# Kernel tuning notes

Hardware: AMD Instinct MI355X
Metric: run time of the kernel (lower is better)

Reference implementation:

```python
import jax, jax.numpy as jnp
import numpy as np

CHUNK = 32
FLOOR = 0.01
EPS_MIX = 1e-5
EPS_NORM = 1e-5


def l2norm(x):
    return x / jnp.sqrt(jnp.sum(x * x, -1, keepdims=True) + 1e-12)


def dw_causal_conv(x, w):
    # x: (B, L, C), w: (C, K) depthwise causal conv, tap K-1 is 'current'
    K = w.shape[-1]
    L = x.shape[1]
    xp = jnp.pad(x, ((0, 0), (K - 1, 0), (0, 0)))
    y = jnp.zeros_like(x)
    for t in range(K):
        y = y + xp[:, t:t + L, :] * w[:, t]
    return y


def delta_rule_chunkwise(q, k, v, beta):
    # q,k: (B,H,L,dk), v: (B,H,L,dv), beta: (B,H,L); L % CHUNK == 0
    b, h, L, dk = q.shape
    dv = v.shape[-1]
    c = CHUNK
    n = L // c
    q = l2norm(q)
    k = l2norm(k)
    v = v * beta[..., None]
    kb = k * beta[..., None]
    rs = lambda x: x.reshape(b, h, n, c, -1)
    qc, kc, vc, kbc = rs(q), rs(k), rs(v), rs(kb)
    # in-chunk inverse of (I + tril(K_beta K^T)) via forward substitution
    T = -jnp.einsum('bhnid,bhnjd->bhnij', kbc, kc)
    tri_strict = jnp.tril(jnp.ones((c, c), bool), -1)
    T = jnp.where(tri_strict, T, 0.0)
    for i in range(1, c):
        T = T.at[..., i, :i].add(
            jnp.einsum('bhnj,bhnji->bhni', T[..., i, :], T[..., :, :i]))
    T = T + jnp.eye(c, dtype=T.dtype)
    u = jnp.einsum('bhnij,bhnjd->bhnid', T, vc)
    w = jnp.einsum('bhnij,bhnjd->bhnid', T, kbc)
    mask_incl = jnp.tril(jnp.ones((c, c), bool), 0)

    def step(S, inp):
        qi, ki, ui, wi = inp  # each (b,h,c,d)
        attn = jnp.einsum('bhid,bhjd->bhij', qi, ki)
        attn = jnp.where(mask_incl, attn, 0.0)
        u_i = ui - jnp.einsum('bhik,bhkd->bhid', wi, S)
        o_i = jnp.einsum('bhik,bhkd->bhid', qi, S) + jnp.einsum('bhij,bhjd->bhid', attn, u_i)
        S = S + jnp.einsum('bhci,bhcd->bhid', ki, u_i)
        return S, o_i

    S0 = jnp.zeros((b, h, dk, dv), q.dtype)
    xs = tuple(jnp.moveaxis(a, 2, 0) for a in (qc, kc, u, w))
    S, o = jax.lax.scan(step, S0, xs)
    o = jnp.moveaxis(o, 0, 2).reshape(b, h, L, dv)
    return o, S


def setup_inputs() -> dict:
    key = jax.random.key(0)
    B, L, D, H = 4, 4096, 1024, 4
    dh = D // H  # 256
    ks = jax.random.split(key, 20)
    s = 1.0 / np.sqrt(D)
    inp = {
        'hidden_states': jax.random.normal(ks[0], (B, L, D), jnp.float32),
        'Wq': jax.random.normal(ks[1], (D, D), jnp.float32) * s,
        'Wk': jax.random.normal(ks[2], (D, D), jnp.float32) * s,
        'Wv': jax.random.normal(ks[3], (D, D), jnp.float32) * s,
        'Wb': jax.random.normal(ks[4], (D, H), jnp.float32) * s,
        'conv_q_w': jax.random.normal(ks[5], (D, 4), jnp.float32) * 0.5,
        'conv_k_w': jax.random.normal(ks[6], (D, 4), jnp.float32) * 0.5,
        'conv_v_w': jax.random.normal(ks[7], (D, 4), jnp.float32) * 0.5,
        'local_w': (jax.random.normal(ks[8], (H * dh, 7), jnp.float32) / np.sqrt(7.0)).at[:, -1].add(1.0),
        'mid_w': (jax.random.normal(ks[9], (H * dh, 25), jnp.float32) / np.sqrt(25.0)).at[:, -1].add(1.0),
        'r_w1': jax.random.normal(ks[10], (D + 14 * H, 2 * (D + 14 * H)), jnp.float32) / np.sqrt(D + 14 * H),
        'r_b1': jnp.zeros((2 * (D + 14 * H),), jnp.float32),
        'r_w2': jax.random.normal(ks[11], (2 * (D + 14 * H), H * 4), jnp.float32) / np.sqrt(2.0 * (D + 14 * H)),
        'r_b2': jnp.zeros((H, 4), jnp.float32).at[:, 2:].set(0.7).reshape(-1),
        'mix_w': jnp.ones((H, dh), jnp.float32),
        'onorm_w': jnp.ones((dh,), jnp.float32),
        'Wo': jax.random.normal(ks[12], (D, D), jnp.float32) * s,
    }
    return inp


def reference(hidden_states, Wq, Wk, Wv, Wb, conv_q_w, conv_k_w, conv_v_w,
              local_w, mid_w, r_w1, r_b1, r_w2, r_b2, mix_w, onorm_w, Wo):
    B, L, D = hidden_states.shape
    H = mix_w.shape[0]
    dh = mix_w.shape[1]
    # projections + short causal depthwise convs with SiLU (qk_activation='silu')
    q = jax.nn.silu(dw_causal_conv(hidden_states @ Wq, conv_q_w))
    k = jax.nn.silu(dw_causal_conv(hidden_states @ Wk, conv_k_w))
    v = jax.nn.silu(dw_causal_conv(hidden_states @ Wv, conv_v_w))
    q4 = q.reshape(B, L, H, dh)
    k4 = k.reshape(B, L, H, dh)
    v4 = v.reshape(B, L, H, dh)
    beta = jax.nn.sigmoid(hidden_states @ Wb)  # (B,L,H)
    delta_out, _ = delta_rule_chunkwise(
        jnp.transpose(q4, (0, 2, 1, 3)), jnp.transpose(k4, (0, 2, 1, 3)),
        jnp.transpose(v4, (0, 2, 1, 3)), jnp.transpose(beta, (0, 2, 1)))
    delta_out = jnp.transpose(delta_out, (0, 2, 1, 3))  # (B,L,H,dh)
    v_direct = v4
    vflat = v4.reshape(B, L, H * dh)
    local_out = dw_causal_conv(vflat, local_w).reshape(B, L, H, dh)
    mid_out = dw_causal_conv(vflat, mid_w).reshape(B, L, H, dh)
    outs = [local_out, mid_out, delta_out, v_direct]
    # router stats: per-head mean/var of each path + pairwise mean dots
    feats = []
    for o_ in outs:
        feats.append(o_.mean(-1))
        feats.append(jnp.var(o_, -1, ddof=1))
    for i in range(4):
        for j in range(i + 1, 4):
            feats.append((outs[i] * outs[j]).mean(-1))
    router_feat = jnp.concatenate([hidden_states] + feats, axis=-1)  # (B,L,D+14H)
    h1 = jax.nn.silu(router_feat @ r_w1 + r_b1)
    logits = (h1 @ r_w2 + r_b2).reshape(B, L, H, 4)
    p = jax.nn.softmax(logits, -1)
    p = p * (1.0 - 4.0 * FLOOR) + FLOOR  # probability floor
    mixed = sum(p[..., i:i + 1] * outs[i] for i in range(4))  # (B,L,H,dh)
    # MixNorm: per-token per-head RMSNorm with (H,dh) affine
    rms = jnp.sqrt(jnp.mean(mixed * mixed, -1, keepdims=True) + EPS_MIX)
    mixed = mixed / rms * mix_w
    # output RMSNorm (per head_v_dim)
    rms2 = jnp.sqrt(jnp.mean(mixed * mixed, -1, keepdims=True) + EPS_NORM)
    o_n = mixed / rms2 * onorm_w
    return o_n.reshape(B, L, H * dh) @ Wo
```

## Files before the change

kernel.cpp:

```cpp
#include <hip/hip_runtime.h>
#include <cstdint>
#include <cstddef>

typedef unsigned short u16;
typedef __bf16 bf16x8 __attribute__((ext_vector_type(8)));
typedef float    f32x4 __attribute__((ext_vector_type(4)));
typedef unsigned short u16x8 __attribute__((ext_vector_type(8)));
typedef unsigned short u16x4 __attribute__((ext_vector_type(4)));

#define MFMA16(a,b,c) __builtin_amdgcn_mfma_f32_16x16x32_bf16(a,b,c,0,0,0)

__device__ __forceinline__ float bf2f(u16 u){ return __uint_as_float(((unsigned)u)<<16); }
__device__ __forceinline__ u16 f2bf(float f){
  unsigned x = __float_as_uint(f);
  unsigned r = x + 0x7fffu + ((x>>16)&1u);
  return (u16)(r>>16);
}
__device__ __forceinline__ float wred(float v){
  #pragma unroll
  for (int o=32;o;o>>=1) v += __shfl_xor(v,o,64);
  return v;
}
__device__ __forceinline__ float siluf(float x){ return x/(1.f+__expf(-x)); }

__global__ __launch_bounds__(256) void k_zero(float* __restrict__ p, int n){
  int i = blockIdx.x*256 + threadIdx.x;
  if (i < n) p[i] = 0.f;
}

__global__ __launch_bounds__(256) void k_cvt(const float* __restrict__ src,
                                             u16* __restrict__ dst, int n){
  int i = (blockIdx.x*256 + threadIdx.x)*4;
  if (i < n){
    float4 f = *(const float4*)(src + i);
    u16x4 o; o[0]=f2bf(f.x); o[1]=f2bf(f.y); o[2]=f2bf(f.z); o[3]=f2bf(f.w);
    *(u16x4*)(dst + i) = o;
  }
}

__global__ __launch_bounds__(256) void k_tr(const float* __restrict__ src, u16* __restrict__ dst,
                                            int R, int C, int Rp, int Cp){
  __shared__ float t[32][33];
  int n0 = blockIdx.x*32, k0 = blockIdx.y*32;
  int tx = threadIdx.x & 31, ty = threadIdx.x >> 5;
  #pragma unroll
  for (int j=0;j<4;j++){
    int k = k0 + ty + j*8, nn = n0 + tx;
    t[ty + j*8][tx] = (k < R && nn < C) ? src[k*C + nn] : 0.f;
  }
  __syncthreads();
  #pragma unroll
  for (int j=0;j<4;j++){
    int nn = n0 + ty + j*8, k = k0 + tx;
    dst[nn*Rp + k] = f2bf(t[tx][ty + j*8]);
  }
}

__global__ __launch_bounds__(256) void k_pad_w2t(const float* __restrict__ src, u16* __restrict__ dst){
  int k = blockIdx.x*256 + threadIdx.x;
  int j = blockIdx.y;
  if (k < 2176) dst[j*2176 + k] = (k < 2160) ? f2bf(src[k*16 + j]) : (u16)0;
}
__global__ __launch_bounds__(256) void k_pad_b1(const float* __restrict__ src, float* __restrict__ dst){
  int i = blockIdx.x*256 + threadIdx.x;
  if (i < 2176) dst[i] = (i<2160) ? src[i] : 0.f;
}

__global__ __launch_bounds__(256,2) void k_gemm(
    const u16* __restrict__ A, const u16* __restrict__ Bt, void* __restrict__ Cvp,
    int M, int N, int K, int out_f32)
{
  __shared__ u16 As[2][128*64];
  __shared__ u16 Bs[2][128*64];
  const int tid = threadIdx.x;
  const int lane = tid & 63, wv = tid >> 6;
  const int wm = (wv>>1)*64, wn = (wv&1)*64;
  const int r15 = lane & 15, q4 = lane >> 4;
  const int bm0 = blockIdx.y*128, bn0 = blockIdx.x*128;
  const int srow = tid>>3, sch = tid&7;
  const int nk = K >> 6;

  const f32x4 fz = {0.f,0.f,0.f,0.f};
  f32x4 acc[4][4];
  #pragma unroll
  for (int i=0;i<4;i++){
    #pragma unroll
    for (int j=0;j<4;j++) acc[i][j] = fz;
  }

  {
    u16x8 ca[4], cb[4];
    #pragma unroll
    for (int i=0;i<4;i++){
      int r = i*32 + srow;
      ca[i] = *(const u16x8*)(A  + (size_t)(bm0+r)*K + sch*8);
      cb[i] = *(const u16x8*)(Bt + (size_t)(bn0+r)*K + sch*8);
    }
    #pragma unroll
    for (int i=0;i<4;i++){
      int r = i*32 + srow;
      int byt = r*128 + ((sch ^ (r&7))*16);
      *(u16x8*)((char*)(&As[0][0]) + byt) = ca[i];
      *(u16x8*)((char*)(&Bs[0][0]) + byt) = cb[i];
    }
  }
  int cur = 0;
  for (int t=0; t<nk; ++t){
    u16x8 na[4], nb[4];
    if (t+1 < nk){
      const int kt = (t+1)<<6;
      #pragma unroll
      for (int i=0;i<4;i++){
        int r = i*32 + srow;
        na[i] = *(const u16x8*)(A  + (size_t)(bm0+r)*K + kt + sch*8);
        nb[i] = *(const u16x8*)(Bt + (size_t)(bn0+r)*K + kt + sch*8);
      }
    }
    __syncthreads();
    const u16* as_ = &As[cur][0];
    const u16* bs_ = &Bs[cur][0];
    #pragma unroll
    for (int kk=0; kk<2; ++kk){
      bf16x8 av[4], bv[4];
      #pragma unroll
      for (int mi=0;mi<4;mi++){
        int row = wm + mi*16 + r15;
        int ch  = kk*4 + q4;
        av[mi] = *(const bf16x8*)((const char*)as_ + row*128 + ((ch ^ (row&7))*16));
      }
      #pragma unroll
      for (int ni=0;ni<4;ni++){
        int row = wn + ni*16 + r15;
        int ch  = kk*4 + q4;
        bv[ni] = *(const bf16x8*)((const char*)bs_ + row*128 + ((ch ^ (row&7))*16));
      }
      #pragma unroll
      for (int mi=0;mi<4;mi++){
        #pragma unroll
        for (int ni=0;ni<4;ni++)
          acc[mi][ni] = MFMA16(av[mi], bv[ni], acc[mi][ni]);
      }
    }
    if (t+1 < nk){
      #pragma unroll
      for (int i=0;i<4;i++){
        int r = i*32 + srow;
        int byt = r*128 + ((sch ^ (r&7))*16);
        *(u16x8*)((char*)(&As[cur^1][0]) + byt) = na[i];
        *(u16x8*)((char*)(&Bs[cur^1][0]) + byt) = nb[i];
      }
    }
    cur ^= 1;
  }
  float* Cf = (float*)Cvp;
  u16*  Cb2 = (u16*)Cvp;
  #pragma unroll
  for (int mi=0;mi<4;mi++){
    #pragma unroll
    for (int ni=0;ni<4;ni++){
      int gr = bm0 + wm + mi*16 + q4*4;
      int gc = bn0 + wn + ni*16 + r15;
      #pragma unroll
      for (int rg=0; rg<4; ++rg){
        float v = acc[mi][ni][rg];
        size_t off = (size_t)(gr+rg)*N + gc;
        if (out_f32) Cf[off] = v; else Cb2[off] = f2bf(v);
      }
    }
  }
}

union SMu {
  struct { u16 As[2][128*64]; u16 Bs[2][128*64]; } g;
  u16 h1s[128][136];
};
__global__ __launch_bounds__(256,2) void k_gemm_router(
    const u16* __restrict__ A, const u16* __restrict__ Bt,
    const float* __restrict__ bias, const u16* __restrict__ w2t,
    float* __restrict__ logits)
{
  __shared__ SMu sm;
  const int tid = threadIdx.x;
  const int lane = tid & 63, wv = tid >> 6;
  const int wm = (wv>>1)*64, wn = (wv&1)*64;
  const int r15 = lane & 15, q4 = lane >> 4;
  const int bm0 = blockIdx.y*128, bn0 = blockIdx.x*128;
  const int srow = tid>>3, sch = tid&7;
  const int K = 1088, nk = 17;

  const f32x4 fz = {0.f,0.f,0.f,0.f};
  f32x4 acc[4][4];
  #pragma unroll
  for (int i=0;i<4;i++){
    #pragma unroll
    for (int j=0;j<4;j++) acc[i][j] = fz;
  }
  {
    u16x8 ca[4], cb[4];
    #pragma unroll
    for (int i=0;i<4;i++){
      int r = i*32 + srow;
      ca[i] = *(const u16x8*)(A  + (size_t)(bm0+r)*K + sch*8);
      cb[i] = *(const u16x8*)(Bt + (size_t)(bn0+r)*K + sch*8);
    }
    #pragma unroll
    for (int i=0;i<4;i++){
      int r = i*32 + srow;
      int byt = r*128 + ((sch ^ (r&7))*16);
      *(u16x8*)((char*)(&sm.g.As[0][0]) + byt) = ca[i];
      *(u16x8*)((char*)(&sm.g.Bs[0][0]) + byt) = cb[i];
    }
  }
  int cur = 0;
  for (int t=0; t<nk; ++t){
    u16x8 na[4], nb[4];
    if (t+1 < nk){
      const int kt = (t+1)<<6;
      #pragma unroll
      for (int i=0;i<4;i++){
        int r = i*32 + srow;
        na[i] = *(const u16x8*)(A  + (size_t)(bm0+r)*K + kt + sch*8);
        nb[i] = *(const u16x8*)(Bt + (size_t)(bn0+r)*K + kt + sch*8);
      }
    }
    __syncthreads();
    const u16* as_ = &sm.g.As[cur][0];
    const u16* bs_ = &sm.g.Bs[cur][0];
    #pragma unroll
    for (int kk=0; kk<2; ++kk){
      bf16x8 av[4], bv[4];
      #pragma unroll
      for (int mi=0;mi<4;mi++){
        int row = wm + mi*16 + r15;
        int ch  = kk*4 + q4;
        av[mi] = *(const bf16x8*)((const char*)as_ + row*128 + ((ch ^ (row&7))*16));
      }
      #pragma unroll
      for (int ni=0;ni<4;ni++){
        int row = wn + ni*16 + r15;
        int ch  = kk*4 + q4;
        bv[ni] = *(const bf16x8*)((const char*)bs_ + row*128 + ((ch ^ (row&7))*16));
      }
      #pragma unroll
      for (int mi=0;mi<4;mi++){
        #pragma unroll
        for (int ni=0;ni<4;ni++)
          acc[mi][ni] = MFMA16(av[mi], bv[ni], acc[mi][ni]);
      }
    }
    if (t+1 < nk){
      #pragma unroll
      for (int i=0;i<4;i++){
        int r = i*32 + srow;
        int byt = r*128 + ((sch ^ (r&7))*16);
        *(u16x8*)((char*)(&sm.g.As[cur^1][0]) + byt) = na[i];
        *(u16x8*)((char*)(&sm.g.Bs[cur^1][0]) + byt) = nb[i];
      }
    }
    cur ^= 1;
  }
  __syncthreads();
  #pragma unroll
  for (int mi=0;mi<4;mi++){
    #pragma unroll
    for (int ni=0;ni<4;ni++){
      int lr = wm + mi*16 + q4*4;
      int lc = wn + ni*16 + r15;
      float bv_ = bias[bn0 + lc];
      #pragma unroll
      for (int rg=0; rg<4; ++rg)
        sm.h1s[lr+rg][lc] = f2bf(siluf(acc[mi][ni][rg] + bv_));
    }
  }
  __syncthreads();
  f32x4 lacc[2] = {fz, fz};
  #pragma unroll
  for (int rt=0; rt<2; ++rt){
    #pragma unroll
    for (int ks=0; ks<4; ++ks){
      bf16x8 a = *(const bf16x8*)((const char*)&sm.h1s[wv*32 + rt*16 + r15][0] + ks*64 + q4*16);
      bf16x8 b = *(const bf16x8*)(w2t + r15*2176 + bn0 + ks*32 + q4*8);
      lacc[rt] = MFMA16(a, b, lacc[rt]);
    }
  }
  #pragma unroll
  for (int rt=0; rt<2; ++rt){
    #pragma unroll
    for (int rg=0; rg<4; ++rg){
      int m = bm0 + wv*32 + rt*16 + q4*4 + rg;
      atomicAdd(&logits[m*16 + r15], lacc[rt][rg]);
    }
  }
}

__global__ __launch_bounds__(256) void k_softm(float* __restrict__ p, const float* __restrict__ b2){
  int m = blockIdx.x*256 + threadIdx.x;
  float l[16];
  #pragma unroll
  for (int j=0;j<16;j++) l[j] = p[m*16+j] + b2[j];
  #pragma unroll
  for (int hh=0;hh<4;hh++){
    float l0=l[hh*4+0], l1=l[hh*4+1], l2=l[hh*4+2], l3=l[hh*4+3];
    float mx = fmaxf(fmaxf(l0,l1),fmaxf(l2,l3));
    float e0=__expf(l0-mx), e1=__expf(l1-mx), e2=__expf(l2-mx), e3=__expf(l3-mx);
    float iv = 1.f/(e0+e1+e2+e3);
    p[m*16+hh*4+0]=e0*iv*0.96f+0.01f;
    p[m*16+hh*4+1]=e1*iv*0.96f+0.01f;
    p[m*16+hh*4+2]=e2*iv*0.96f+0.01f;
    p[m*16+hh*4+3]=e3*iv*0.96f+0.01f;
  }
}

__global__ __launch_bounds__(256) void k_beta(const u16* __restrict__ Xb,
                                              const float* __restrict__ Wb,
                                              float* __restrict__ beta){
  int m = blockIdx.x*4 + (threadIdx.x>>6);
  int lane = threadIdx.x & 63;
  float a0=0.f,a1=0.f,a2=0.f,a3=0.f;
  #pragma unroll 4
  for (int i=0;i<16;i++){
    int k = lane + i*64;
    float x = bf2f(Xb[m*1024 + k]);
    float4 wr = *(const float4*)(Wb + k*4);
    a0 += x*wr.x; a1 += x*wr.y; a2 += x*wr.z; a3 += x*wr.w;
  }
  a0 = wred(a0); a1 = wred(a1); a2 = wred(a2); a3 = wred(a3);
  if (lane == 0){
    beta[m*4+0] = 1.f/(1.f+__expf(-a0));
    beta[m*4+1] = 1.f/(1.f+__expf(-a1));
    beta[m*4+2] = 1.f/(1.f+__expf(-a2));
    beta[m*4+3] = 1.f/(1.f+__expf(-a3));
  }
}

__global__ __launch_bounds__(256) void k_conv(const u16* __restrict__ raw,
                                              const float* __restrict__ cw,
                                              u16* __restrict__ outp, int do_norm){
  const int m = blockIdx.x;
  const int tid = threadIdx.x, lane = tid&63, hh = tid>>6;
  const int l = m & 4095;
  const int cbase = hh*256 + lane*4;
  float x[4][4];
  #pragma unroll
  for (int j=0;j<4;j++){
    if (l >= j){
      u16x4 xv = *(const u16x4*)(raw + (m-j)*1024 + cbase);
      #pragma unroll
      for (int e=0;e<4;e++) x[j][e] = bf2f(xv[e]);
    } else {
      #pragma unroll
      for (int e=0;e<4;e++) x[j][e] = 0.f;
    }
  }
  float y[4]; float ss = 0.f;
  #pragma unroll
  for (int e=0;e<4;e++){
    int c = cbase + e;
    float yy = x[0][e]*cw[c*4+3] + x[1][e]*cw[c*4+2] + x[2][e]*cw[c*4+1] + x[3][e]*cw[c*4+0];
    yy = siluf(yy);
    y[e] = yy; ss += yy*yy;
  }
  if (do_norm){
    ss = wred(ss);
    float sc = rsqrtf(ss + 1e-12f);
    #pragma unroll
    for (int e=0;e<4;e++) y[e] *= sc;
  }
  u16x4 o;
  #pragma unroll
  for (int e=0;e<4;e++) o[e] = f2bf(y[e]);
  *(u16x4*)(outp + m*1024 + cbase) = o;
}

__global__ __launch_bounds__(256) void k_localmid(const u16* __restrict__ v,
                                                  const float* __restrict__ lw,
                                                  const float* __restrict__ mw,
                                                  u16* __restrict__ lo, u16* __restrict__ mo){
  __shared__ u16 vs[56][256];
  const int lt0 = blockIdx.x*32;
  const int b = blockIdx.y;
  const int c0 = blockIdx.z*256;
  const int tid = threadIdx.x;
  #pragma unroll
  for (int i=0;i<7;i++){
    int flat = tid + i*256;
    int row = flat >> 5;
    int cc = (flat & 31)*8;
    int tok = lt0 - 24 + row;
    u16x8 val = {0,0,0,0,0,0,0,0};
    if (tok >= 0) val = *(const u16x8*)(v + (b*4096 + tok)*1024 + c0 + cc);
    *(u16x8*)&vs[row][cc] = val;
  }
  __syncthreads();
  const int c = tid;
  float lwr[7], mwr[25];
  #pragma unroll
  for (int i=0;i<7;i++) lwr[i] = lw[(c0+c)*7 + i];
  #pragma unroll
  for (int i=0;i<25;i++) mwr[i] = mw[(c0+c)*25 + i];
  for (int lt=0; lt<32; ++lt){
    float a7=0.f, a25=0.f;
    #pragma unroll
    for (int t=0;t<25;t++) a25 += bf2f(vs[lt+t][c]) * mwr[t];
    #pragma unroll
    for (int t=0;t<7;t++)  a7  += bf2f(vs[18+lt+t][c]) * lwr[t];
    int m = b*4096 + lt0 + lt;
    lo[m*1024 + c0 + c] = f2bf(a7);
    mo[m*1024 + c0 + c] = f2bf(a25);
  }
}

__global__ __launch_bounds__(256,2) void k_chunk(
    const u16* __restrict__ qn, const u16* __restrict__ kn, const u16* __restrict__ v,
    const float* __restrict__ beta, u16* __restrict__ u_, u16* __restrict__ w_,
    u16* __restrict__ attnb)
{
  const int chk = blockIdx.x;
  const int nc = chk & 127;
  const int bh = chk >> 7;
  const int b = bh >> 2, h = bh & 3;
  const int tok0 = b*4096 + nc*32;
  const int tid = threadIdx.x, lane = tid&63, wv = tid>>6;
  const int r15 = lane&15, q4 = lane>>4;

  __shared__ u16 kbT[256][40];
  __shared__ u16 vbT[256][40];
  __shared__ float Tm[4][32][33];
  __shared__ u16 Xs[32][40];

  {
    int rr = tid >> 3;
    int cb = (tid & 7)*32;
    float bt = beta[(tok0 + rr)*4 + h];
    const u16* ksrc = kn + (tok0+rr)*1024 + h*256 + cb;
    const u16* vsrc = v  + (tok0+rr)*1024 + h*256 + cb;
    #pragma unroll
    for (int vvv=0; vvv<4; ++vvv){
      u16x8 kx = *(const u16x8*)(ksrc + vvv*8);
      u16x8 vx = *(const u16x8*)(vsrc + vvv*8);
      #pragma unroll
      for (int e=0;e<8;e++){
        kbT[cb + vvv*8 + e][rr] = f2bf(bf2f(kx[e]) * bt);
        vbT[cb + vvv*8 + e][rr] = f2bf(bf2f(vx[e]) * bt);
      }
    }
  }
  {
    const int i0 = (wv>>1)*16, j0 = (wv&1)*16;
    float bi = beta[(tok0 + i0 + r15)*4 + h];
    f32x4 tacc = {0.f,0.f,0.f,0.f};
    #pragma unroll
    for (int ks=0; ks<8; ++ks){
      u16x8 ar = *(const u16x8*)(kn + (tok0 + i0 + r15)*1024 + h*256 + ks*32 + q4*8);
      union { u16x8 u; bf16x8 bf; } au;
      #pragma unroll
      for (int e=0;e<8;e++) au.u[e] = f2bf(bf2f(ar[e]) * bi);
      bf16x8 bv = *(const bf16x8*)(kn + (tok0 + j0 + r15)*1024 + h*256 + ks*32 + q4*8);
      tacc = MFMA16(au.bf, bv, tacc);
    }
    #pragma unroll
    for (int rg=0; rg<4; ++rg){
      int i = i0 + q4*4 + rg, j = j0 + r15;
      float val = (i > j) ? -tacc[rg] : 0.f;
      Tm[0][i][j] = val;
      Tm[2][i][j] = val + ((i==j)?1.f:0.f);
    }
  }
  __syncthreads();
  int cbuf = 0, cx = 2;
  const int ii = tid >> 3, jj = (tid&7)*4;
  for (int s=0; s<4; ++s){
    int nb = cbuf^1, nx = cx^1;
    {
      float o0=0.f,o1=0.f,o2=0.f,o3=0.f;
      for (int k=0;k<32;k++){
        float a = Tm[cbuf][ii][k];
        o0 += a*Tm[cbuf][k][jj+0]; o1 += a*Tm[cbuf][k][jj+1];
        o2 += a*Tm[cbuf][k][jj+2]; o3 += a*Tm[cbuf][k][jj+3];
      }
      Tm[nb][ii][jj+0]=o0; Tm[nb][ii][jj+1]=o1; Tm[nb][ii][jj+2]=o2; Tm[nb][ii][jj+3]=o3;
    }
    __syncthreads();
    {
      float o0=Tm[cx][ii][jj+0], o1=Tm[cx][ii][jj+1], o2=Tm[cx][ii][jj+2], o3=Tm[cx][ii][jj+3];
      for (int k=0;k<32;k++){
        float a = Tm[nb][ii][k];
        o0 += a*Tm[cx][k][jj+0]; o1 += a*Tm[cx][k][jj+1];
        o2 += a*Tm[cx][k][jj+2]; o3 += a*Tm[cx][k][jj+3];
      }
      Tm[nx][ii][jj+0]=o0; Tm[nx][ii][jj+1]=o1; Tm[nx][ii][jj+2]=o2; Tm[nx][ii][jj+3]=o3;
    }
    __syncthreads();
    cbuf = nb; cx = nx;
  }
  {
    #pragma unroll
    for (int e=0;e<4;e++) Xs[ii][jj+e] = f2bf(Tm[cx][ii][jj+e]);
  }
  __syncthreads();
  {
    #pragma unroll
    for (int nt=0; nt<4; ++nt){
      int n0 = wv*64 + nt*16;
      #pragma unroll
      for (int mt=0; mt<2; ++mt){
        bf16x8 a = *(const bf16x8*)((const char*)&Xs[mt*16 + r15][0] + q4*16);
        bf16x8 bu = *(const bf16x8*)((const char*)&vbT[n0 + r15][0] + q4*16);
        bf16x8 bw = *(const bf16x8*)((const char*)&kbT[n0 + r15][0] + q4*16);
        f32x4 ua = {0.f,0.f,0.f,0.f};
        f32x4 wa = {0.f,0.f,0.f,0.f};
        ua = MFMA16(a, bu, ua);
        wa = MFMA16(a, bw, wa);
        #pragma unroll
        for (int rg=0;rg<4;rg++){
          int row = mt*16 + q4*4 + rg;
          int col = n0 + r15;
          u_[(chk*32 + row)*256 + col] = f2bf(ua[rg]);
          w_[(chk*32 + row)*256 + col] = f2bf(wa[rg]);
        }
      }
    }
  }
  {
    const int i0 = (wv>>1)*16, j0 = (wv&1)*16;
    f32x4 aacc = {0.f,0.f,0.f,0.f};
    #pragma unroll
    for (int ks=0;ks<8;++ks){
      bf16x8 a = *(const bf16x8*)(qn + (tok0 + i0 + r15)*1024 + h*256 + ks*32 + q4*8);
      bf16x8 bv = *(const bf16x8*)(kn + (tok0 + j0 + r15)*1024 + h*256 + ks*32 + q4*8);
      aacc = MFMA16(a, bv, aacc);
    }
    #pragma unroll
    for (int rg=0;rg<4;rg++){
      int i = i0 + q4*4 + rg, j = j0 + r15;
      attnb[chk*1024 + i*32 + j] = f2bf((i>=j)? aacc[rg] : 0.f);
    }
  }
}

__global__ __launch_bounds__(256,1) void k_scan(
    const u16* __restrict__ qn, const u16* __restrict__ kn,
    const u16* __restrict__ u_, const u16* __restrict__ w_,
    const u16* __restrict__ attnb, u16* __restrict__ od)
{
  const int bid = blockIdx.x;
  const int bh = bid >> 3;
  const int b = bh >> 2, h = bh & 3;
  const int dv0 = (bid & 7)*32;
  const int tid = threadIdx.x, lane = tid & 63, wv = tid >> 6;
  const int tm = wv >> 1, tn = wv & 1;
  const int r15 = lane & 15, q4 = lane >> 4;

  __shared__ u16 SbT[32][264];
  __shared__ u16 knT[2][256][40];
  __shared__ u16 uT[32][40];

  for (int i = tid; i < 32*264; i += 256) (&SbT[0][0])[i] = 0;
  const f32x4 fz = {0.f,0.f,0.f,0.f};
  f32x4 Sacc[4][2];
  #pragma unroll
  for (int a_=0;a_<4;a_++){
    #pragma unroll
    for (int b_=0;b_<2;b_++) Sacc[a_][b_] = fz;
  }
  const int srr = tid >> 3, scb = (tid & 7)*32;
  {
    const u16* src = kn + (b*4096 + srr)*1024 + h*256 + scb;
    #pragma unroll
    for (int vvv=0; vvv<4; ++vvv){
      u16x8 x = *(const u16x8*)(src + vvv*8);
      #pragma unroll
      for (int e=0;e<8;e++) knT[0][scb+vvv*8+e][srr] = x[e];
    }
  }
  __syncthreads();

  for (int nc = 0; nc < 128; ++nc){
    const int kb_ = nc & 1;
    const int tok0 = b*4096 + nc*32;
    const int chk = bh*128 + nc;
    if (nc+1 < 128){
      const u16* src = kn + (tok0 + 32 + srr)*1024 + h*256 + scb;
      #pragma unroll
      for (int vvv=0; vvv<4; ++vvv){
        u16x8 x = *(const u16x8*)(src + vvv*8);
        #pragma unroll
        for (int e=0;e<8;e++) knT[kb_^1][scb+vvv*8+e][srr] = x[e];
      }
    }
    f32x4 ua0 = fz, ua1 = fz;
    const u16* wrow = w_ + (chk*32 + tm*16 + r15)*256;
    #pragma unroll
    for (int ks=0; ks<8; ks+=2){
      bf16x8 a0 = *(const bf16x8*)(wrow + ks*32 + q4*8);
      bf16x8 s0 = *(const bf16x8*)((const char*)&SbT[tn*16 + r15][0] + ks*64 + q4*16);
      ua0 = MFMA16(a0, s0, ua0);
      bf16x8 a1 = *(const bf16x8*)(wrow + (ks+1)*32 + q4*8);
      bf16x8 s1 = *(const bf16x8*)((const char*)&SbT[tn*16 + r15][0] + (ks+1)*64 + q4*16);
      ua1 = MFMA16(a1, s1, ua1);
    }
    const u16* ubp = u_ + (chk*32 + tm*16)*256 + dv0 + tn*16;
    #pragma unroll
    for (int rg=0; rg<4; ++rg){
      float uiv = bf2f(ubp[(q4*4+rg)*256 + r15]) - ua0[rg] - ua1[rg];
      uT[tn*16 + r15][tm*16 + q4*4 + rg] = f2bf(uiv);
    }
    __syncthreads();

    f32x4 oa0 = fz, oa1 = fz;
    const u16* qrow = qn + (tok0 + tm*16 + r15)*1024 + h*256;
    #pragma unroll
    for (int ks=0; ks<8; ks+=2){
      bf16x8 a0 = *(const bf16x8*)(qrow + ks*32 + q4*8);
      bf16x8 s0 = *(const bf16x8*)((const char*)&SbT[tn*16 + r15][0] + ks*64 + q4*16);
      oa0 = MFMA16(a0, s0, oa0);
      bf16x8 a1 = *(const bf16x8*)(qrow + (ks+1)*32 + q4*8);
      bf16x8 s1 = *(const bf16x8*)((const char*)&SbT[tn*16 + r15][0] + (ks+1)*64 + q4*16);
      oa1 = MFMA16(a1, s1, oa1);
    }
    {
      bf16x8 a = *(const bf16x8*)(attnb + chk*1024 + (tm*16 + r15)*32 + q4*8);
      bf16x8 bu = *(const bf16x8*)((const char*)&uT[tn*16 + r15][0] + q4*16);
      oa0 = MFMA16(a, bu, oa0);
    }
    #pragma unroll
    for (int rg=0;rg<4;rg++)
      od[(tok0 + tm*16 + q4*4 + rg)*1024 + h*256 + dv0 + tn*16 + r15] = f2bf(oa0[rg] + oa1[rg]);

    #pragma unroll
    for (int mt=0; mt<4; ++mt){
      bf16x8 a = *(const bf16x8*)((const char*)&knT[kb_][wv*64 + mt*16 + r15][0] + q4*16);
      #pragma unroll
      for (int ntl=0; ntl<2; ++ntl){
        bf16x8 bu = *(const bf16x8*)((const char*)&uT[ntl*16 + r15][0] + q4*16);
        Sacc[mt][ntl] = MFMA16(a, bu, Sacc[mt][ntl]);
      }
    }
    __syncthreads();
    #pragma unroll
    for (int mt=0; mt<4; ++mt){
      #pragma unroll
      for (int ntl=0; ntl<2; ++ntl){
        #pragma unroll
        for (int rg=0; rg<4; ++rg)
          SbT[ntl*16 + r15][wv*64 + mt*16 + q4*4 + rg] = f2bf(Sacc[mt][ntl][rg]);
      }
    }
    __syncthreads();
  }
}

__global__ __launch_bounds__(256) void k_feats(
    const float* __restrict__ Xf, const u16* __restrict__ lo, const u16* __restrict__ mo,
    const u16* __restrict__ de, const u16* __restrict__ vv, u16* __restrict__ feat)
{
  const int m = blockIdx.x;
  const int tid = threadIdx.x, lane = tid & 63, hh = tid >> 6;
  {
    float4 xv = *(const float4*)(Xf + m*1024 + tid*4);
    u16x4 o; o[0]=f2bf(xv.x); o[1]=f2bf(xv.y); o[2]=f2bf(xv.z); o[3]=f2bf(xv.w);
    *(u16x4*)(feat + m*1088 + tid*4) = o;
  }
  if (tid < 8) feat[m*1088 + 1080 + tid] = 0;
  const int base = m*1024 + hh*256 + lane*4;
  u16x4 a0 = *(const u16x4*)(lo + base);
  u16x4 a1 = *(const u16x4*)(mo + base);
  u16x4 a2 = *(const u16x4*)(de + base);
  u16x4 a3 = *(const u16x4*)(vv + base);
  float s[14];
  #pragma unroll
  for (int i=0;i<14;i++) s[i]=0.f;
  #pragma unroll
  for (int e=0;e<4;e++){
    float L = bf2f(a0[e]), Mm = bf2f(a1[e]), D = bf2f(a2[e]), V = bf2f(a3[e]);
    s[0]+=L; s[1]+=L*L; s[2]+=Mm; s[3]+=Mm*Mm; s[4]+=D; s[5]+=D*D; s[6]+=V; s[7]+=V*V;
    s[8]+=L*Mm; s[9]+=L*D; s[10]+=L*V; s[11]+=Mm*D; s[12]+=Mm*V; s[13]+=D*V;
  }
  #pragma unroll
  for (int i=0;i<14;i++) s[i] = wred(s[i]);
  if (lane == 0){
    const float inv = 1.f/256.f, invv = 1.f/255.f;
    u16* fb = feat + m*1088 + 1024;
    float mn[4] = {s[0]*inv, s[2]*inv, s[4]*inv, s[6]*inv};
    float vr[4] = {(s[1]-256.f*mn[0]*mn[0])*invv, (s[3]-256.f*mn[1]*mn[1])*invv,
                   (s[5]-256.f*mn[2]*mn[2])*invv, (s[7]-256.f*mn[3]*mn[3])*invv};
    #pragma unroll
    for (int i=0;i<4;i++){ fb[(2*i)*4 + hh] = f2bf(mn[i]); fb[(2*i+1)*4 + hh] = f2bf(vr[i]); }
    #pragma unroll
    for (int i=0;i<6;i++) fb[(8+i)*4 + hh] = f2bf(s[8+i]*inv);
  }
}

__global__ __launch_bounds__(256) void k_mix(
    const u16* __restrict__ lo, const u16* __restrict__ mo, const u16* __restrict__ de,
    const u16* __restrict__ vv, const float* __restrict__ p,
    const float* __restrict__ mixw, const float* __restrict__ onw, u16* __restrict__ on)
{
  const int m = blockIdx.x;
  const int tid = threadIdx.x, lane = tid&63, hh = tid>>6;
  const int dbase = lane*4;
  const int base = m*1024 + hh*256 + dbase;
  float4 pv = *(const float4*)(p + m*16 + hh*4);
  u16x4 a0 = *(const u16x4*)(lo + base);
  u16x4 a1 = *(const u16x4*)(mo + base);
  u16x4 a2 = *(const u16x4*)(de + base);
  u16x4 a3 = *(const u16x4*)(vv + base);
  float g[4]; float ss = 0.f;
  #pragma unroll
  for (int e=0;e<4;e++){
    float x = pv.x*bf2f(a0[e]) + pv.y*bf2f(a1[e]) + pv.z*bf2f(a2[e]) + pv.w*bf2f(a3[e]);
    g[e]=x; ss += x*x;
  }
  ss = wred(ss);
  float r1 = rsqrtf(ss*(1.f/256.f) + 1e-5f);
  float ss2 = 0.f;
  #pragma unroll
  for (int e=0;e<4;e++){ g[e] = g[e]*r1*mixw[hh*256 + dbase + e]; ss2 += g[e]*g[e]; }
  ss2 = wred(ss2);
  float r2 = rsqrtf(ss2*(1.f/256.f) + 1e-5f);
  u16x4 o;
  #pragma unroll
  for (int e=0;e<4;e++) o[e] = f2bf(g[e]*r2*onw[dbase + e]);
  *(u16x4*)(on + base) = o;
}

extern "C" void kernel_launch(void* const* d_in, const int* in_sizes, int n_in,
                              void* d_out, int out_size, void* d_ws, size_t ws_size,
                              hipStream_t stream)
{
  const float* X   = (const float*)d_in[0];
  const float* Wq  = (const float*)d_in[1];
  const float* Wk  = (const float*)d_in[2];
  const float* Wv  = (const float*)d_in[3];
  const float* Wb  = (const float*)d_in[4];
  const float* cqw = (const float*)d_in[5];
  const float* ckw = (const float*)d_in[6];
  const float* cvw = (const float*)d_in[7];
  const float* lw  = (const float*)d_in[8];
  const float* mw  = (const float*)d_in[9];
  const float* rw1 = (const float*)d_in[10];
  const float* rb1 = (const float*)d_in[11];
  const float* rw2 = (const float*)d_in[12];
  const float* rb2 = (const float*)d_in[13];
  const float* mixw= (const float*)d_in[14];
  const float* onw = (const float*)d_in[15];
  const float* Wo  = (const float*)d_in[16];

  char* ws = (char*)d_ws;
  const size_t SLOT = 33554432;
  char* s0 = ws;
  char* s1 = ws + 1*SLOT;
  char* s2 = ws + 2*SLOT;
  char* s3 = ws + 3*SLOT;
  char* s4 = ws + 4*SLOT;
  char* s5 = ws + 5*SLOT;
  char* ext = ws + 6*SLOT;
  u16*   attb  = (u16*)(ext);
  float* pb    = (float*)(ext + 4194304);
  float* betab = (float*)(ext + 4194304 + 1048576);
  char*  wsp   = ext + 4194304 + 1048576 + 262144;
  u16* Wqt = (u16*)(wsp);
  u16* Wkt = (u16*)(wsp + 2097152);
  u16* Wvt = (u16*)(wsp + 2*2097152);
  u16* Wot = (u16*)(wsp + 3*2097152);
  u16* w1t = (u16*)(wsp + 4*2097152);
  u16* w2t = (u16*)(wsp + 4*2097152 + 4734976);
  float* b1p = (float*)(wsp + 4*2097152 + 4734976 + 69632);

  u16* Xb    = (u16*)s0;
  u16* rawb  = (u16*)s1;
  u16* qnb   = (u16*)s2;
  u16* knb   = (u16*)s3;
  u16* vpb   = (u16*)s4;
  u16* ub    = (u16*)s0;
  u16* wbuf  = (u16*)s1;
  u16* odb   = (u16*)s5;
  u16* lob   = (u16*)s2;
  u16* mob   = (u16*)s3;
  u16* featb = (u16*)s0;
  u16* onb   = (u16*)s0;

  k_zero<<<1024,256,0,stream>>>(pb, 262144);
  k_cvt<<<16384,256,0,stream>>>(X, Xb, 16777216);
  k_tr<<<dim3(32,32),256,0,stream>>>(Wq, Wqt, 1024,1024,1024,1024);
  k_tr<<<dim3(32,32),256,0,stream>>>(Wk, Wkt, 1024,1024,1024,1024);
  k_tr<<<dim3(32,32),256,0,stream>>>(Wv, Wvt, 1024,1024,1024,1024);
  k_tr<<<dim3(32,32),256,0,stream>>>(Wo, Wot, 1024,1024,1024,1024);
  k_tr<<<dim3(68,34),256,0,stream>>>(rw1, w1t, 1080,2160,1088,2176);
  k_pad_w2t<<<dim3(9,16),256,0,stream>>>(rw2, w2t);
  k_pad_b1<<<9,256,0,stream>>>(rb1, b1p);
  k_gemm<<<dim3(8,128),256,0,stream>>>(Xb, Wqt, rawb, 16384,1024,1024, 0);
  k_conv<<<16384,256,0,stream>>>(rawb, cqw, qnb, 1);
  k_gemm<<<dim3(8,128),256,0,stream>>>(Xb, Wkt, rawb, 16384,1024,1024, 0);
  k_conv<<<16384,256,0,stream>>>(rawb, ckw, knb, 1);
  k_gemm<<<dim3(8,128),256,0,stream>>>(Xb, Wvt, rawb, 16384,1024,1024, 0);
  k_conv<<<16384,256,0,stream>>>(rawb, cvw, vpb, 0);
  k_beta<<<4096,256,0,stream>>>(Xb, Wb, betab);
  k_chunk<<<2048,256,0,stream>>>(qnb, knb, vpb, betab, ub, wbuf, attb);
  k_scan<<<128,256,0,stream>>>(qnb, knb, ub, wbuf, attb, odb);
  k_localmid<<<dim3(128,4,4),256,0,stream>>>(vpb, lw, mw, lob, mob);
  k_feats<<<16384,256,0,stream>>>(X, lob, mob, odb, vpb, featb);
  k_gemm_router<<<dim3(17,128),256,0,stream>>>(featb, w1t, b1p, w2t, pb);
  k_softm<<<64,256,0,stream>>>(pb, rb2);
  k_mix<<<16384,256,0,stream>>>(lob, mob, odb, vpb, pb, mixw, onw, onb);
  k_gemm<<<dim3(8,128),256,0,stream>>>(onb, Wot, d_out, 16384,1024,1024, 1);
}
```

Baseline: 1.207 ms.

## Pre-transpose K per chunk and software-pipeline the delta-rule scan with double-buffered state

Adds a separate kernel that writes K transposed per chunk into a workspace buffer, so the serial scan can load it with vector stores instead of scalar transposed LDS writes. The scan loop is unrolled by two with a macro that double-buffers the LDS state matrix and the K tile. It prefetches the next chunk's W and K, and the current chunk's Q, attention and u, into registers ahead of use, which also removes one barrier per chunk. The cost is an extra kernel launch, an extra 32 MB workspace slot with its global traffic, and higher register pressure in the scan.

After: 1.250 ms. 1.04x slower.

```diff
diff --git a/kernel.cpp b/kernel.cpp
--- a/kernel.cpp
+++ b/kernel.cpp
@@ -64,6 +64,30 @@
 __global__ __launch_bounds__(256) void k_pad_b1(const float* __restrict__ src, float* __restrict__ dst){
   int i = blockIdx.x*256 + threadIdx.x;
   if (i < 2176) dst[i] = (i<2160) ? src[i] : 0.f;
+}
+
+__global__ __launch_bounds__(256) void k_trk(const u16* __restrict__ kn, u16* __restrict__ kTb){
+  __shared__ u16 vs[32][264];
+  const int g = blockIdx.x;
+  const int bh = g >> 7, nc = g & 127;
+  const int b = bh >> 2, h = bh & 3;
+  const int tid = threadIdx.x;
+  const int rr = tid >> 3, cb = (tid & 7) * 32;
+  const u16* src = kn + (size_t)(b*4096 + nc*32 + rr)*1024 + h*256 + cb;
+  #pragma unroll
+  for (int v=0; v<4; ++v){
+    u16x8 x = *(const u16x8*)(src + v*8);
+    *(u16x8*)&vs[rr][cb + v*8] = x;
+  }
+  __syncthreads();
+  u16* dst = kTb + ((size_t)g*256 + tid)*32;
+  #pragma unroll
+  for (int v=0; v<4; ++v){
+    u16x8 o;
+    #pragma unroll
+    for (int e=0; e<8; e++) o[e] = vs[v*8 + e][tid];
+    *(u16x8*)(dst + v*8) = o;
+  }
 }
 
 __global__ __launch_bounds__(256,2) void k_gemm(
@@ -538,8 +562,56 @@
   }
 }
 
+#define SCAN_BODY(NC, WCUR, WNXT, CB, NB) { \
+  const int chk_ = bh*128 + (NC); \
+  const int ncn_ = ((NC)+1 < 128) ? (NC)+1 : 127; \
+  const int chkn_ = bh*128 + ncn_; \
+  u16x8 kst[4]; \
+  { const u16* kc = kTb + (size_t)chkn_*8192 + tid*32; \
+    _Pragma("unroll") for (int v=0;v<4;++v) kst[v] = *(const u16x8*)(kc + v*8); } \
+  _Pragma("unroll") for (int ks=0;ks<8;++ks) \
+    WNXT[ks] = *(const u16x8*)(w_ + (size_t)(chkn_*32 + tm*16 + r15)*256 + ks*32 + q4*8); \
+  u16x8 qv[8]; \
+  _Pragma("unroll") for (int ks=0;ks<8;++ks) \
+    qv[ks] = *(const u16x8*)(qn + (size_t)(b*4096 + (NC)*32 + tm*16 + r15)*1024 + h*256 + ks*32 + q4*8); \
+  u16x8 atv = *(const u16x8*)(attnb + (size_t)chk_*1024 + (tm*16 + r15)*32 + q4*8); \
+  u16 uvv[4]; \
+  _Pragma("unroll") for (int rg=0;rg<4;++rg) \
+    uvv[rg] = u_[(size_t)(chk_*32 + tm*16 + q4*4 + rg)*256 + dv0 + tn*16 + r15]; \
+  f32x4 ua = fz, ub2 = fz; \
+  _Pragma("unroll") for (int ks=0;ks<8;ks+=2){ \
+    bf16x8 s0 = *(const bf16x8*)((const char*)&Sb[CB][tn*16 + r15][0] + ks*64 + q4*16); \
+    ua = MFMA16(*(const bf16x8*)&WCUR[ks], s0, ua); \
+    bf16x8 s1 = *(const bf16x8*)((const char*)&Sb[CB][tn*16 + r15][0] + (ks+1)*64 + q4*16); \
+    ub2 = MFMA16(*(const bf16x8*)&WCUR[ks+1], s1, ub2); } \
+  _Pragma("unroll") for (int rg=0;rg<4;++rg){ \
+    float uiv = bf2f(uvv[rg]) - ua[rg] - ub2[rg]; \
+    uT[tn*16 + r15][tm*16 + q4*4 + rg] = f2bf(uiv); } \
+  __syncthreads(); \
+  f32x4 oa = fz, ob = fz; \
+  _Pragma("unroll") for (int ks=0;ks<8;ks+=2){ \
+    bf16x8 s0 = *(const bf16x8*)((const char*)&Sb[CB][tn*16 + r15][0] + ks*64 + q4*16); \
+    oa = MFMA16(*(const bf16x8*)&qv[ks], s0, oa); \
+    bf16x8 s1 = *(const bf16x8*)((const char*)&Sb[CB][tn*16 + r15][0] + (ks+1)*64 + q4*16); \
+    ob = MFMA16(*(const bf16x8*)&qv[ks+1], s1, ob); } \
+  { bf16x8 bu = *(const bf16x8*)((const char*)&uT[tn*16 + r15][0] + q4*16); \
+    oa = MFMA16(*(const bf16x8*)&atv, bu, oa); } \
+  _Pragma("unroll") for (int rg=0;rg<4;++rg) \
+    od[(size_t)(b*4096 + (NC)*32 + tm*16 + q4*4 + rg)*1024 + h*256 + dv0 + tn*16 + r15] = f2bf(oa[rg] + ob[rg]); \
+  _Pragma("unroll") for (int mt=0;mt<4;++mt){ \
+    bf16x8 a = *(const bf16x8*)((const char*)&knT[CB][wv*64 + mt*16 + r15][0] + q4*16); \
+    _Pragma("unroll") for (int ntl=0;ntl<2;++ntl){ \
+      bf16x8 bu = *(const bf16x8*)((const char*)&uT[ntl*16 + r15][0] + q4*16); \
+      Sacc[mt][ntl] = MFMA16(a, bu, Sacc[mt][ntl]); } } \
+  _Pragma("unroll") for (int mt=0;mt<4;++mt) \
+    _Pragma("unroll") for (int ntl=0;ntl<2;++ntl) \
+      _Pragma("unroll") for (int rg=0;rg<4;++rg) \
+        Sb[NB][ntl*16 + r15][wv*64 + mt*16 + q4*4 + rg] = f2bf(Sacc[mt][ntl][rg]); \
+  _Pragma("unroll") for (int v=0;v<4;++v) *(u16x8*)(&knT[NB][tid][0] + v*8) = kst[v]; \
+  __syncthreads(); }
+
 __global__ __launch_bounds__(256,1) void k_scan(
-    const u16* __restrict__ qn, const u16* __restrict__ kn,
+    const u16* __restrict__ qn, const u16* __restrict__ kTb,
     const u16* __restrict__ u_, const u16* __restrict__ w_,
     const u16* __restrict__ attnb, u16* __restrict__ od)
 {
@@ -551,11 +623,11 @@
   const int tm = wv >> 1, tn = wv & 1;
   const int r15 = lane & 15, q4 = lane >> 4;
 
-  __shared__ u16 SbT[32][264];
-  __shared__ u16 knT[2][256][40];
-  __shared__ u16 uT[32][40];
-
-  for (int i = tid; i < 32*264; i += 256) (&SbT[0][0])[i] = 0;
+  __shared__ u16 Sb[2][32][264];
+  __shared__ u16 knT[2][256][36];
+  __shared__ u16 uT[32][36];
+
+  for (int i = tid; i < 32*264; i += 256) (&Sb[0][0][0])[i] = 0;
   const f32x4 fz = {0.f,0.f,0.f,0.f};
   f32x4 Sacc[4][2];
   #pragma unroll
@@ -563,90 +635,23 @@
     #pragma unroll
     for (int b_=0;b_<2;b_++) Sacc[a_][b_] = fz;
   }
-  const int srr = tid >> 3, scb = (tid & 7)*32;
   {
-    const u16* src = kn + (b*4096 + srr)*1024 + h*256 + scb;
-    #pragma unroll
-    for (int vvv=0; vvv<4; ++vvv){
-      u16x8 x = *(const u16x8*)(src + vvv*8);
-      #pragma unroll
-      for (int e=0;e<8;e++) knT[0][scb+vvv*8+e][srr] = x[e];
-    }
-  }
+    const u16* kc = kTb + (size_t)(bh*128)*8192 + tid*32;
+    u16x8 k0[4];
+    #pragma unroll
+    for (int v=0;v<4;++v) k0[v] = *(const u16x8*)(kc + v*8);
+    #pragma unroll
+    for (int v=0;v<4;++v) *(u16x8*)(&knT[0][tid][0] + v*8) = k0[v];
+  }
+  u16x8 wA[8], wB[8];
+  #pragma unroll
+  for (int ks=0;ks<8;++ks)
+    wA[ks] = *(const u16x8*)(w_ + (size_t)((bh*128)*32 + tm*16 + r15)*256 + ks*32 + q4*8);
   __syncthreads();
 
-  for (int nc = 0; nc < 128; ++nc){
-    const int kb_ = nc & 1;
-    const int tok0 = b*4096 + nc*32;
-    const int chk = bh*128 + nc;
-    if (nc+1 < 128){
-      const u16* src = kn + (tok0 + 32 + srr)*1024 + h*256 + scb;
-      #pragma unroll
-      for (int vvv=0; vvv<4; ++vvv){
-        u16x8 x = *(const u16x8*)(src + vvv*8);
-        #pragma unroll
-        for (int e=0;e<8;e++) knT[kb_^1][scb+vvv*8+e][srr] = x[e];
-      }
-    }
-    f32x4 ua0 = fz, ua1 = fz;
-    const u16* wrow = w_ + (chk*32 + tm*16 + r15)*256;
-    #pragma unroll
-    for (int ks=0; ks<8; ks+=2){
-      bf16x8 a0 = *(const bf16x8*)(wrow + ks*32 + q4*8);
-      bf16x8 s0 = *(const bf16x8*)((const char*)&SbT[tn*16 + r15][0] + ks*64 + q4*16);
-      ua0 = MFMA16(a0, s0, ua0);
-      bf16x8 a1 = *(const bf16x8*)(wrow + (ks+1)*32 + q4*8);
-      bf16x8 s1 = *(const bf16x8*)((const char*)&SbT[tn*16 + r15][0] + (ks+1)*64 + q4*16);
-      ua1 = MFMA16(a1, s1, ua1);
-    }
-    const u16* ubp = u_ + (chk*32 + tm*16)*256 + dv0 + tn*16;
-    #pragma unroll
-    for (int rg=0; rg<4; ++rg){
-      float uiv = bf2f(ubp[(q4*4+rg)*256 + r15]) - ua0[rg] - ua1[rg];
-      uT[tn*16 + r15][tm*16 + q4*4 + rg] = f2bf(uiv);
-    }
-    __syncthreads();
-
-    f32x4 oa0 = fz, oa1 = fz;
-    const u16* qrow = qn + (tok0 + tm*16 + r15)*1024 + h*256;
-    #pragma unroll
-    for (int ks=0; ks<8; ks+=2){
-      bf16x8 a0 = *(const bf16x8*)(qrow + ks*32 + q4*8);
-      bf16x8 s0 = *(const bf16x8*)((const char*)&SbT[tn*16 + r15][0] + ks*64 + q4*16);
-      oa0 = MFMA16(a0, s0, oa0);
-      bf16x8 a1 = *(const bf16x8*)(qrow + (ks+1)*32 + q4*8);
-      bf16x8 s1 = *(const bf16x8*)((const char*)&SbT[tn*16 + r15][0] + (ks+1)*64 + q4*16);
-      oa1 = MFMA16(a1, s1, oa1);
-    }
-    {
-      bf16x8 a = *(const bf16x8*)(attnb + chk*1024 + (tm*16 + r15)*32 + q4*8);
-      bf16x8 bu = *(const bf16x8*)((const char*)&uT[tn*16 + r15][0] + q4*16);
-      oa0 = MFMA16(a, bu, oa0);
-    }
-    #pragma unroll
-    for (int rg=0;rg<4;rg++)
-      od[(tok0 + tm*16 + q4*4 + rg)*1024 + h*256 + dv0 + tn*16 + r15] = f2bf(oa0[rg] + oa1[rg]);
-
-    #pragma unroll
-    for (int mt=0; mt<4; ++mt){
-      bf16x8 a = *(const bf16x8*)((const char*)&knT[kb_][wv*64 + mt*16 + r15][0] + q4*16);
-      #pragma unroll
-      for (int ntl=0; ntl<2; ++ntl){
-        bf16x8 bu = *(const bf16x8*)((const char*)&uT[ntl*16 + r15][0] + q4*16);
-        Sacc[mt][ntl] = MFMA16(a, bu, Sacc[mt][ntl]);
-      }
-    }
-    __syncthreads();
-    #pragma unroll
-    for (int mt=0; mt<4; ++mt){
-      #pragma unroll
-      for (int ntl=0; ntl<2; ++ntl){
-        #pragma unroll
-        for (int rg=0; rg<4; ++rg)
-          SbT[ntl*16 + r15][wv*64 + mt*16 + q4*4 + rg] = f2bf(Sacc[mt][ntl][rg]);
-      }
-    }
-    __syncthreads();
+  for (int nc = 0; nc < 128; nc += 2){
+    SCAN_BODY(nc,   wA, wB, 0, 1)
+    SCAN_BODY(nc+1, wB, wA, 1, 0)
   }
 }
 
@@ -754,7 +759,8 @@
   char* s3 = ws + 3*SLOT;
   char* s4 = ws + 4*SLOT;
   char* s5 = ws + 5*SLOT;
-  char* ext = ws + 6*SLOT;
+  char* s6 = ws + 6*SLOT;
+  char* ext = ws + 7*SLOT;
   u16*   attb  = (u16*)(ext);
   float* pb    = (float*)(ext + 4194304);
   float* betab = (float*)(ext + 4194304 + 1048576);
@@ -775,6 +781,7 @@
   u16* ub    = (u16*)s0;
   u16* wbuf  = (u16*)s1;
   u16* odb   = (u16*)s5;
+  u16* kTbp  = (u16*)s6;
   u16* lob   = (u16*)s2;
   u16* mob   = (u16*)s3;
   u16* featb = (u16*)s0;
@@ -797,7 +804,8 @@
   k_conv<<<16384,256,0,stream>>>(rawb, cvw, vpb, 0);
   k_beta<<<4096,256,0,stream>>>(Xb, Wb, betab);
   k_chunk<<<2048,256,0,stream>>>(qnb, knb, vpb, betab, ub, wbuf, attb);
-  k_scan<<<128,256,0,stream>>>(qnb, knb, ub, wbuf, attb, odb);
+  k_trk<<<2048,256,0,stream>>>(knb, kTbp);
+  k_scan<<<128,256,0,stream>>>(qnb, kTbp, ub, wbuf, attb, odb);
   k_localmid<<<dim3(128,4,4),256,0,stream>>>(vpb, lw, mw, lob, mob);
   k_feats<<<16384,256,0,stream>>>(X, lob, mob, odb, vpb, featb);
   k_gemm_router<<<dim3(17,128),256,0,stream>>>(featb, w1t, b1p, w2t, pb);
```
